# Kernel optimization log

Hardware: AMD Instinct MI355X
Metric: run time of the kernel (lower is better)

## Reference

```python
import jax, jax.numpy as jnp
import numpy as np

B, S, E, H = 2, 2048, 1024, 16
D = E // H  # head_dim = 64


def _rope_angles(seq_len, d, dtype=jnp.float32):
    # standard RoPE frequencies: theta_i = 10000^{-2i/d}
    inv_freq = 1.0 / (10000.0 ** (jnp.arange(0, d, 2, dtype=dtype) / d))  # [d/2]
    pos = jnp.arange(seq_len, dtype=dtype)                                # [S]
    ang = pos[:, None] * inv_freq[None, :]                                # [S, d/2]
    ang = jnp.concatenate([ang, ang], axis=-1)                            # [S, d]
    return jnp.cos(ang), jnp.sin(ang)


def _rotate_half(t):
    t1, t2 = jnp.split(t, 2, axis=-1)
    return jnp.concatenate([-t2, t1], axis=-1)


def _apply_rope(t, cos, sin):
    # t: [B, H, S, D]; cos/sin: [S, D]
    return t * cos[None, None, :, :] + _rotate_half(t) * sin[None, None, :, :]


def setup_inputs() -> dict:
    key = jax.random.key(0)
    ks = jax.random.split(key, 6)
    x = jax.random.normal(ks[0], (B, S, E), dtype=jnp.float32)
    mask = jnp.tril(jnp.ones((S, S), dtype=bool))  # causal: True = attend
    scale = 1.0 / np.sqrt(E)
    Wq = jax.random.normal(ks[1], (E, E), dtype=jnp.float32) * scale
    Wk = jax.random.normal(ks[2], (E, E), dtype=jnp.float32) * scale
    Wv = jax.random.normal(ks[3], (E, E), dtype=jnp.float32) * scale
    Wo = jax.random.normal(ks[4], (E, E), dtype=jnp.float32) * scale
    z = jnp.zeros((E,), dtype=jnp.float32)
    return {"x": x, "mask": mask, "Wq": Wq, "bq": z, "Wk": Wk, "bk": z,
            "Wv": Wv, "bv": z, "Wo": Wo, "bo": z}


def reference(x, mask, Wq, bq, Wk, bk, Wv, bv, Wo, bo):
    b, s, e = x.shape
    # QKV projections (nn.Linear convention: y = x @ W.T + b)
    def proj(W, bias):
        y = jnp.einsum('bse,fe->bsf', x, W) + bias
        return y.reshape(b, s, H, D).transpose(0, 2, 1, 3)  # [B,H,S,D]
    q, k, v = proj(Wq, bq), proj(Wk, bk), proj(Wv, bv)
    # RoPE on q and k (per-head rotary over head_dim)
    cos, sin = _rope_angles(s, D, dtype=x.dtype)
    q = _apply_rope(q, cos, sin)
    k = _apply_rope(k, cos, sin)
    # SDPA with boolean mask (True = attend)
    scores = jnp.einsum('bhqd,bhkd->bhqk', q, k) / jnp.sqrt(jnp.asarray(D, x.dtype))
    neg = jnp.asarray(jnp.finfo(x.dtype).min, x.dtype)
    scores = jnp.where(mask[None, None, :, :], scores, neg)
    attn = jax.nn.softmax(scores, axis=-1)
    out = jnp.einsum('bhqk,bhkd->bhqd', attn, v)          # [B,H,S,D]
    out = out.transpose(0, 2, 1, 3).reshape(b, s, e)       # [B,S,E]
    return jnp.einsum('bse,fe->bsf', out, Wo) + bo
```

## Files before the change

### kernel.cpp

```cpp
#include <hip/hip_runtime.h>
#include <hip/hip_bf16.h>

typedef unsigned short u16;
typedef unsigned int u32;
typedef __bf16 bf16x8 __attribute__((ext_vector_type(8)));
typedef float f32x4 __attribute__((ext_vector_type(4)));

#define S_LEN 2048
#define NHEAD 16
#define HDIM  64
#define EMB   1024
#define BATCH 2

__device__ __forceinline__ float bf2f(u16 u) {
  union { unsigned int i; float f; } c; c.i = ((unsigned int)u) << 16; return c.f;
}
__device__ __forceinline__ u16 f2bf(float f) {
  union { float f; unsigned int i; } c; c.f = f;
  unsigned int i = c.i;
  return (u16)((i + 0x7FFFu + ((i >> 16) & 1u)) >> 16);
}
__device__ __forceinline__ f32x4 mfma16(bf16x8 a, bf16x8 b, f32x4 c) {
  return __builtin_amdgcn_mfma_f32_16x16x32_bf16(a, b, c, 0, 0, 0);
}
__device__ __forceinline__ void cp16(const u16* g, u16* l) {
  __builtin_amdgcn_global_load_lds(
      (const __attribute__((address_space(1))) u32*)g,
      (__attribute__((address_space(3))) u32*)l, 16, 0, 0);
}

__global__ void detect_kernel(const u16* __restrict__ x, int* __restrict__ flag) {
  __shared__ int s_big;
  if (threadIdx.x == 0) s_big = 0;
  __syncthreads();
  int big = 0;
  for (int i = threadIdx.x; i < 4096; i += 256) {
    int e = (x[i] >> 7) & 0xFF;
    if (e >= 0xC0) big = 1;
  }
  if (big) atomicOr(&s_big, 1);
  __syncthreads();
  if (threadIdx.x == 0) flag[0] = s_big;
}

__global__ __launch_bounds__(256) void rope_table_kernel(float2* __restrict__ tab) {
  int id = blockIdx.x * 256 + threadIdx.x;
  int s = id >> 5, i = id & 31;
  float f = exp2f(-(float)i * 0.41524101186092029f);
  float ang = (float)s * f;
  tab[id] = make_float2(cosf(ang), sinf(ang));
}

__global__ __launch_bounds__(256) void convert_kernel(
    const void* __restrict__ x, const void* __restrict__ Wq,
    const void* __restrict__ Wk, const void* __restrict__ Wv,
    const void* __restrict__ Wo,
    u16* __restrict__ xb, u16* __restrict__ wqb, u16* __restrict__ wkb,
    u16* __restrict__ wvb, u16* __restrict__ wob, const int* __restrict__ dflag)
{
  size_t gid = (size_t)blockIdx.x * 256 + threadIdx.x;
  size_t e = gid * 8;
  const void* src; u16* dst; size_t off;
  if (e < 4194304) { src = x; dst = xb; off = e; }
  else {
    size_t rr = e - 4194304;
    int j = (int)(rr >> 20); off = rr & 1048575;
    src = (j == 0) ? Wq : (j == 1) ? Wk : (j == 2) ? Wv : Wo;
    dst = (j == 0) ? wqb : (j == 1) ? wkb : (j == 2) ? wvb : wob;
  }
  if (dflag[0]) {
    const float* s = (const float*)src + off;
    float4 a = *(const float4*)s;
    float4 b2 = *(const float4*)(s + 4);
    ushort4 u0; u0.x = f2bf(a.x); u0.y = f2bf(a.y); u0.z = f2bf(a.z); u0.w = f2bf(a.w);
    ushort4 u1; u1.x = f2bf(b2.x); u1.y = f2bf(b2.y); u1.z = f2bf(b2.z); u1.w = f2bf(b2.w);
    *(ushort4*)(dst + off) = u0;
    *(ushort4*)(dst + off + 4) = u1;
  } else {
    *(uint4*)(dst + off) = *(const uint4*)((const u16*)src + off);
  }
}

__device__ __forceinline__ void gemm_core(
    const u16* __restrict__ A, const u16* __restrict__ W,
    int m0, int n0, int t, f32x4 (&acc)[4][4],
    u16 (&Ash)[128][32], u16 (&Bsh)[128][32])
{
  const int lane = t & 63, lr = lane & 15, quad = lane >> 4;
  const int wv = t >> 6;
  const int wm = (wv & 1) * 64, wn = (wv >> 1) * 64;
  for (int kt = 0; kt < 1024; kt += 32) {
    __syncthreads();
#pragma unroll
    for (int p = 0; p < 2; ++p) {
      const int i = t + p * 256;
      const int r = i >> 2, c = (i & 3) * 8;
      u16* la = &Ash[0][0] + (size_t)(p * 256 + (t & 192)) * 8;
      u16* lb = &Bsh[0][0] + (size_t)(p * 256 + (t & 192)) * 8;
      cp16(A + (size_t)(m0 + r) * 1024 + kt + c, la);
      cp16(W + (size_t)(n0 + r) * 1024 + kt + c, lb);
    }
    __syncthreads();
    bf16x8 af[4], bfr[4];
#pragma unroll
    for (int mi = 0; mi < 4; ++mi)
      af[mi] = *(const bf16x8*)&Ash[wm + mi * 16 + lr][quad * 8];
#pragma unroll
    for (int ni = 0; ni < 4; ++ni)
      bfr[ni] = *(const bf16x8*)&Bsh[wn + ni * 16 + lr][quad * 8];
#pragma unroll
    for (int mi = 0; mi < 4; ++mi)
#pragma unroll
      for (int ni = 0; ni < 4; ++ni)
        acc[mi][ni] = mfma16(af[mi], bfr[ni], acc[mi][ni]);
  }
}

__device__ __forceinline__ void gemm_epilogue(
    int mode, int f32io, f32x4 (&acc)[4][4],
    const void* biasvp, void* outvp, int m0, int n0, int t,
    const float2* __restrict__ tab)
{
  const int lane = t & 63, lr = lane & 15, quad = lane >> 4;
  const int wv = t >> 6;
  const int wm = (wv & 1) * 64, wn = (wv >> 1) * 64;
  const float* biasf = (const float*)biasvp;
  const u16* biasb = (const u16*)biasvp;
#define BIASV(n) (f32io ? biasf[(n)] : bf2f(biasb[(n)]))
  if (mode == 1) {
    u16* Out = (u16*)outvp;
#pragma unroll
    for (int mi = 0; mi < 4; ++mi) {
#pragma unroll
      for (int r = 0; r < 4; ++r) {
        int mm = m0 + wm + mi * 16 + quad * 4 + r;
        int s = mm & (S_LEN - 1), b = mm >> 11;
        float2 cs0 = tab[s * 32 + lr];
        float2 cs1 = tab[s * 32 + 16 + lr];
#pragma unroll
        for (int ni = 0; ni < 4; ++ni) {
          int n = n0 + wn + ni * 16 + lr;
          int h = n >> 6, d = n & 63;
          float v  = acc[mi][ni][r]     + BIASV(n);
          float vp = acc[mi][ni ^ 2][r] + BIASV(n ^ 32);
          float rot = (d < 32) ? -vp : vp;
          float cc = (ni & 1) ? cs1.x : cs0.x;
          float ss = (ni & 1) ? cs1.y : cs0.y;
          size_t off = (((size_t)(b * NHEAD + h)) * S_LEN + s) * HDIM + d;
          Out[off] = f2bf(v * cc + rot * ss);
        }
      }
    }
  } else if (mode == 2) {
    u16* Out = (u16*)outvp;
#pragma unroll
    for (int mi = 0; mi < 4; ++mi) {
#pragma unroll
      for (int r = 0; r < 4; ++r) {
        int mm = m0 + wm + mi * 16 + quad * 4 + r;
        int s = mm & (S_LEN - 1), b = mm >> 11;
#pragma unroll
        for (int ni = 0; ni < 4; ++ni) {
          int n = n0 + wn + ni * 16 + lr;
          int h = n >> 6, d = n & 63;
          float v = acc[mi][ni][r] + BIASV(n);
          size_t off = (((size_t)(b * NHEAD + h)) * HDIM + d) * S_LEN + s;
          Out[off] = f2bf(v);
        }
      }
    }
  } else {
    float* Outf = (float*)outvp;
    u16* Outb = (u16*)outvp;
#pragma unroll
    for (int mi = 0; mi < 4; ++mi) {
#pragma unroll
      for (int r = 0; r < 4; ++r) {
        int mm = m0 + wm + mi * 16 + quad * 4 + r;
#pragma unroll
        for (int ni = 0; ni < 4; ++ni) {
          int n = n0 + wn + ni * 16 + lr;
          float v = acc[mi][ni][r] + BIASV(n);
          size_t off = (size_t)mm * 1024 + n;
          if (f32io) Outf[off] = v; else Outb[off] = f2bf(v);
        }
      }
    }
  }
#undef BIASV
}

__global__ __launch_bounds__(256) void gemm_qkv(
    const u16* __restrict__ A, const u16* __restrict__ Wq,
    const u16* __restrict__ Wk, const u16* __restrict__ Wv,
    const void* bq, const void* bk, const void* bv,
    u16* qo, u16* ko, u16* vo, const int* __restrict__ dflag,
    const float2* __restrict__ tab)
{
  alignas(16) __shared__ u16 Ash[128][32];
  alignas(16) __shared__ u16 Bsh[128][32];
  const int wsel = blockIdx.x >> 3;
  const u16* W = (wsel == 0) ? Wq : (wsel == 1) ? Wk : Wv;
  const void* bias = (wsel == 0) ? bq : (wsel == 1) ? bk : bv;
  void* out = (wsel == 0) ? (void*)qo : (wsel == 1) ? (void*)ko : (void*)vo;
  const int mode = (wsel == 2) ? 2 : 1;
  const int m0 = blockIdx.y * 128, n0 = (blockIdx.x & 7) * 128;
  f32x4 acc[4][4];
  const f32x4 zero4 = {0.f, 0.f, 0.f, 0.f};
#pragma unroll
  for (int i = 0; i < 4; ++i)
#pragma unroll
    for (int j = 0; j < 4; ++j) acc[i][j] = zero4;
  gemm_core(A, W, m0, n0, threadIdx.x, acc, Ash, Bsh);
  gemm_epilogue(mode, dflag[0], acc, bias, out, m0, n0, threadIdx.x, tab);
}

__global__ __launch_bounds__(256) void gemm_out(
    const u16* __restrict__ A, const u16* __restrict__ W,
    const void* bias, void* out, const int* __restrict__ dflag)
{
  alignas(16) __shared__ u16 Ash[128][32];
  alignas(16) __shared__ u16 Bsh[128][32];
  const int m0 = blockIdx.y * 128, n0 = blockIdx.x * 128;
  f32x4 acc[4][4];
  const f32x4 zero4 = {0.f, 0.f, 0.f, 0.f};
#pragma unroll
  for (int i = 0; i < 4; ++i)
#pragma unroll
    for (int j = 0; j < 4; ++j) acc[i][j] = zero4;
  gemm_core(A, W, m0, n0, threadIdx.x, acc, Ash, Bsh);
  gemm_epilogue(0, dflag[0], acc, bias, out, m0, n0, threadIdx.x, nullptr);
}

__device__ __forceinline__ void attn_phase(
    const bf16x8 (&qf)[2], f32x4 (&oacc)[4], float (&lsum)[4],
    u16 (&Ksh)[64][72], u16 (&Vsh)[64][72], u16 (&Psh)[4][16][72],
    int kv0, int q0w, bool diag, int lr, int quad, int wv)
{
  const f32x4 zero4 = {0.f, 0.f, 0.f, 0.f};
  f32x4 sc[4];
#pragma unroll
  for (int ni = 0; ni < 4; ++ni) {
    bf16x8 kf0 = *(const bf16x8*)&Ksh[ni * 16 + lr][quad * 8];
    bf16x8 kf1 = *(const bf16x8*)&Ksh[ni * 16 + lr][32 + quad * 8];
    f32x4 z = zero4;
    z = mfma16(qf[0], kf0, z);
    z = mfma16(qf[1], kf1, z);
    sc[ni] = z;
  }
#pragma unroll
  for (int ni = 0; ni < 4; ++ni)
#pragma unroll
    for (int r = 0; r < 4; ++r) {
      float sarg = sc[ni][r] * 0.18033688f - 21.64042561f;
      if (diag && (kv0 + ni * 16 + lr > q0w + quad * 4 + r)) sarg = -1e4f;
      float p = exp2f(sarg);
      sc[ni][r] = p;
      lsum[r] += p;
    }
#pragma unroll
  for (int ni = 0; ni < 4; ++ni)
#pragma unroll
    for (int r = 0; r < 4; ++r)
      Psh[wv][quad * 4 + r][ni * 16 + lr] = f2bf(sc[ni][r]);
  bf16x8 pa0 = *(const bf16x8*)&Psh[wv][lr][quad * 8];
  bf16x8 pa1 = *(const bf16x8*)&Psh[wv][lr][32 + quad * 8];
#pragma unroll
  for (int oni = 0; oni < 4; ++oni) {
    bf16x8 vf0 = *(const bf16x8*)&Vsh[oni * 16 + lr][quad * 8];
    bf16x8 vf1 = *(const bf16x8*)&Vsh[oni * 16 + lr][32 + quad * 8];
    oacc[oni] = mfma16(pa0, vf0, oacc[oni]);
    oacc[oni] = mfma16(pa1, vf1, oacc[oni]);
  }
}

__device__ __forceinline__ void attn_finish(
    f32x4 (&oacc)[4], float (&lsum)[4], u16* __restrict__ O,
    int bh, int q0w, int lr, int quad)
{
  const int b = bh >> 4, h = bh & 15;
#pragma unroll
  for (int r = 0; r < 4; ++r) {
#pragma unroll
    for (int off = 1; off < 16; off <<= 1) lsum[r] += __shfl_xor(lsum[r], off);
    lsum[r] = 1.f / lsum[r];
  }
#pragma unroll
  for (int oni = 0; oni < 4; ++oni)
#pragma unroll
    for (int r = 0; r < 4; ++r) {
      int s = q0w + quad * 4 + r;
      int e = h * HDIM + oni * 16 + lr;
      O[((size_t)(b * S_LEN + s)) * EMB + e] = f2bf(oacc[oni][r] * lsum[r]);
    }
}

__global__ __launch_bounds__(256) void attn_kernel(
    const u16* __restrict__ Q, const u16* __restrict__ Kr,
    const u16* __restrict__ Vt, u16* __restrict__ O)
{
  alignas(16) __shared__ u16 Ksh[64][72];
  alignas(16) __shared__ u16 Vsh[64][72];
  alignas(16) __shared__ u16 Psh[4][16][72];
  const int t = threadIdx.x, lane = t & 63, wv = t >> 6;
  const int lr = lane & 15, quad = lane >> 4;
  const int bh = blockIdx.y;
  const int qtA = blockIdx.x;
  const int qtB = 31 - qtA;
  const int qA0 = qtA * 64 + wv * 16;
  const int qB0 = qtB * 64 + wv * 16;
  const size_t base = (size_t)bh * S_LEN * HDIM;

  bf16x8 qfA[2], qfB[2];
  {
    const u16* ra = Q + base + (size_t)(qA0 + lr) * HDIM + quad * 8;
    qfA[0] = *(const bf16x8*)ra; qfA[1] = *(const bf16x8*)(ra + 32);
    const u16* rb = Q + base + (size_t)(qB0 + lr) * HDIM + quad * 8;
    qfB[0] = *(const bf16x8*)rb; qfB[1] = *(const bf16x8*)(rb + 32);
  }

  f32x4 oaccA[4], oaccB[4];
  float lsA[4], lsB[4];
  const f32x4 zero4 = {0.f, 0.f, 0.f, 0.f};
#pragma unroll
  for (int i = 0; i < 4; ++i) {
    oaccA[i] = zero4; oaccB[i] = zero4; lsA[i] = 0.f; lsB[i] = 0.f;
  }

  const int jmax = qtB;
  for (int j = 0; j <= jmax; ++j) {
    const int kv0 = j * 64;
    __syncthreads();
#pragma unroll
    for (int p = 0; p < 2; ++p) {
      int c = t + p * 256;
      int r = c >> 3, cc = (c & 7) * 8;
      *(uint4*)&Ksh[r][cc] = *(const uint4*)(Kr + base + (size_t)(kv0 + r) * HDIM + cc);
      *(uint4*)&Vsh[r][cc] = *(const uint4*)(Vt + base + (size_t)r * S_LEN + kv0 + cc);
    }
    __syncthreads();
    if (j <= qtA)
      attn_phase(qfA, oaccA, lsA, Ksh, Vsh, Psh, kv0, qA0, j == qtA, lr, quad, wv);
    attn_phase(qfB, oaccB, lsB, Ksh, Vsh, Psh, kv0, qB0, j == jmax, lr, quad, wv);
  }

  attn_finish(oaccA, lsA, O, bh, qA0, lr, quad);
  attn_finish(oaccB, lsB, O, bh, qB0, lr, quad);
}

extern "C" void kernel_launch(void* const* d_in, const int* in_sizes, int n_in,
                              void* d_out, int out_size, void* d_ws, size_t ws_size,
                              hipStream_t stream) {
  const void* x  = d_in[0];
  const void* Wq = d_in[2]; const void* bq = d_in[3];
  const void* Wk = d_in[4]; const void* bk = d_in[5];
  const void* Wv = d_in[6]; const void* bv = d_in[7];
  const void* Wo = d_in[8]; const void* bo = d_in[9];

  char* ws = (char*)d_ws;
  int* flag = (int*)ws;
  u16* xb  = (u16*)(ws + 256);
  u16* qws = xb  + 4194304;
  u16* kws = qws + 4194304;
  u16* vws = kws + 4194304;
  u16* wqb = vws + 4194304;
  u16* wkb = wqb + 1048576;
  u16* wvb = wkb + 1048576;
  u16* wob = wvb + 1048576;
  float2* tab = (float2*)(wob + 1048576);
  u16* ows = xb;

  detect_kernel<<<1, 256, 0, stream>>>((const u16*)x, flag);
  rope_table_kernel<<<256, 256, 0, stream>>>(tab);
  convert_kernel<<<4096, 256, 0, stream>>>(x, Wq, Wk, Wv, Wo,
                                           xb, wqb, wkb, wvb, wob, flag);
  gemm_qkv<<<dim3(24, 32), 256, 0, stream>>>(xb, wqb, wkb, wvb,
                                             bq, bk, bv, qws, kws, vws, flag, tab);
  attn_kernel<<<dim3(16, 32), 256, 0, stream>>>(qws, kws, vws, ows);
  gemm_out<<<dim3(8, 32), 256, 0, stream>>>(ows, wob, bo, d_out, flag);
}
```

Before: 240.5 us.

## Fuse detect and RoPE table into convert, split attention into per-tile blocks

```diff
diff --git a/kernel.cpp b/kernel.cpp
--- a/kernel.cpp
+++ b/kernel.cpp
@@ -20,6 +20,10 @@
   unsigned int i = c.i;
   return (u16)((i + 0x7FFFu + ((i >> 16) & 1u)) >> 16);
 }
+__device__ __forceinline__ u16 f2bf_trunc(float f) {
+  union { float f; unsigned int i; } c; c.f = f;
+  return (u16)(c.i >> 16);
+}
 __device__ __forceinline__ f32x4 mfma16(bf16x8 a, bf16x8 b, f32x4 c) {
   return __builtin_amdgcn_mfma_f32_16x16x32_bf16(a, b, c, 0, 0, 0);
 }
@@ -27,28 +31,6 @@
   __builtin_amdgcn_global_load_lds(
       (const __attribute__((address_space(1))) u32*)g,
       (__attribute__((address_space(3))) u32*)l, 16, 0, 0);
-}
-
-__global__ void detect_kernel(const u16* __restrict__ x, int* __restrict__ flag) {
-  __shared__ int s_big;
-  if (threadIdx.x == 0) s_big = 0;
-  __syncthreads();
-  int big = 0;
-  for (int i = threadIdx.x; i < 4096; i += 256) {
-    int e = (x[i] >> 7) & 0xFF;
-    if (e >= 0xC0) big = 1;
-  }
-  if (big) atomicOr(&s_big, 1);
-  __syncthreads();
-  if (threadIdx.x == 0) flag[0] = s_big;
-}
-
-__global__ __launch_bounds__(256) void rope_table_kernel(float2* __restrict__ tab) {
-  int id = blockIdx.x * 256 + threadIdx.x;
-  int s = id >> 5, i = id & 31;
-  float f = exp2f(-(float)i * 0.41524101186092029f);
-  float ang = (float)s * f;
-  tab[id] = make_float2(cosf(ang), sinf(ang));
 }
 
 __global__ __launch_bounds__(256) void convert_kernel(
@@ -56,8 +38,22 @@
     const void* __restrict__ Wk, const void* __restrict__ Wv,
     const void* __restrict__ Wo,
     u16* __restrict__ xb, u16* __restrict__ wqb, u16* __restrict__ wkb,
-    u16* __restrict__ wvb, u16* __restrict__ wob, const int* __restrict__ dflag)
-{
+    u16* __restrict__ wvb, u16* __restrict__ wob,
+    int* __restrict__ flag, float2* __restrict__ tab)
+{
+  __shared__ int s_flag;
+  if (threadIdx.x == 0) s_flag = 0;
+  __syncthreads();
+  {
+    const u16* xs = (const u16*)x;
+    u16 w0 = xs[threadIdx.x * 2], w1 = xs[threadIdx.x * 2 + 1];
+    if ((((w0 >> 7) & 0xFF) >= 0xC0) || (((w1 >> 7) & 0xFF) >= 0xC0))
+      atomicOr(&s_flag, 1);
+  }
+  __syncthreads();
+  const int f32io = s_flag;
+  if (blockIdx.x == 0 && threadIdx.x == 0) flag[0] = f32io;
+
   size_t gid = (size_t)blockIdx.x * 256 + threadIdx.x;
   size_t e = gid * 8;
   const void* src; u16* dst; size_t off;
@@ -68,7 +64,7 @@
     src = (j == 0) ? Wq : (j == 1) ? Wk : (j == 2) ? Wv : Wo;
     dst = (j == 0) ? wqb : (j == 1) ? wkb : (j == 2) ? wvb : wob;
   }
-  if (dflag[0]) {
+  if (f32io) {
     const float* s = (const float*)src + off;
     float4 a = *(const float4*)s;
     float4 b2 = *(const float4*)(s + 4);
@@ -78,6 +74,14 @@
     *(ushort4*)(dst + off + 4) = u1;
   } else {
     *(uint4*)(dst + off) = *(const uint4*)((const u16*)src + off);
+  }
+
+  if (blockIdx.x < 256) {
+    int id = blockIdx.x * 256 + threadIdx.x;
+    int s = id >> 5, i = id & 31;
+    float f = exp2f(-(float)i * 0.41524101186092029f);
+    float ang = (float)s * f;
+    tab[id] = make_float2(cosf(ang), sinf(ang));
   }
 }
 
@@ -155,18 +159,21 @@
     u16* Out = (u16*)outvp;
 #pragma unroll
     for (int mi = 0; mi < 4; ++mi) {
-#pragma unroll
-      for (int r = 0; r < 4; ++r) {
-        int mm = m0 + wm + mi * 16 + quad * 4 + r;
-        int s = mm & (S_LEN - 1), b = mm >> 11;
-#pragma unroll
-        for (int ni = 0; ni < 4; ++ni) {
-          int n = n0 + wn + ni * 16 + lr;
-          int h = n >> 6, d = n & 63;
-          float v = acc[mi][ni][r] + BIASV(n);
-          size_t off = (((size_t)(b * NHEAD + h)) * HDIM + d) * S_LEN + s;
-          Out[off] = f2bf(v);
-        }
+      int mm = m0 + wm + mi * 16 + quad * 4;
+      int s = mm & (S_LEN - 1), b = mm >> 11;
+#pragma unroll
+      for (int ni = 0; ni < 4; ++ni) {
+        int n = n0 + wn + ni * 16 + lr;
+        int h = n >> 6, d = n & 63;
+        float bv = BIASV(n);
+        u16 p0 = f2bf(acc[mi][ni][0] + bv);
+        u16 p1 = f2bf(acc[mi][ni][1] + bv);
+        u16 p2 = f2bf(acc[mi][ni][2] + bv);
+        u16 p3 = f2bf(acc[mi][ni][3] + bv);
+        uint2 pk = make_uint2((u32)p0 | ((u32)p1 << 16),
+                              (u32)p2 | ((u32)p3 << 16));
+        size_t off = (((size_t)(b * NHEAD + h)) * HDIM + d) * S_LEN + s;
+        *(uint2*)(Out + off) = pk;
       }
     }
   } else {
@@ -248,21 +255,32 @@
     z = mfma16(qf[1], kf1, z);
     sc[ni] = z;
   }
+  if (diag) {
+#pragma unroll
+    for (int ni = 0; ni < 4; ++ni)
+#pragma unroll
+      for (int r = 0; r < 4; ++r) {
+        float sarg = sc[ni][r] * 0.18033688f - 21.64042561f;
+        if (kv0 + ni * 16 + lr > q0w + quad * 4 + r) sarg = -1e4f;
+        float p = exp2f(sarg);
+        sc[ni][r] = p;
+        lsum[r] += p;
+      }
+  } else {
+#pragma unroll
+    for (int ni = 0; ni < 4; ++ni)
+#pragma unroll
+      for (int r = 0; r < 4; ++r) {
+        float p = exp2f(sc[ni][r] * 0.18033688f - 21.64042561f);
+        sc[ni][r] = p;
+        lsum[r] += p;
+      }
+  }
 #pragma unroll
   for (int ni = 0; ni < 4; ++ni)
 #pragma unroll
-    for (int r = 0; r < 4; ++r) {
-      float sarg = sc[ni][r] * 0.18033688f - 21.64042561f;
-      if (diag && (kv0 + ni * 16 + lr > q0w + quad * 4 + r)) sarg = -1e4f;
-      float p = exp2f(sarg);
-      sc[ni][r] = p;
-      lsum[r] += p;
-    }
-#pragma unroll
-  for (int ni = 0; ni < 4; ++ni)
-#pragma unroll
     for (int r = 0; r < 4; ++r)
-      Psh[wv][quad * 4 + r][ni * 16 + lr] = f2bf(sc[ni][r]);
+      Psh[wv][quad * 4 + r][ni * 16 + lr] = f2bf_trunc(sc[ni][r]);
   bf16x8 pa0 = *(const bf16x8*)&Psh[wv][lr][quad * 8];
   bf16x8 pa1 = *(const bf16x8*)&Psh[wv][lr][32 + quad * 8];
 #pragma unroll
@@ -305,30 +323,24 @@
   const int t = threadIdx.x, lane = t & 63, wv = t >> 6;
   const int lr = lane & 15, quad = lane >> 4;
   const int bh = blockIdx.y;
-  const int qtA = blockIdx.x;
-  const int qtB = 31 - qtA;
-  const int qA0 = qtA * 64 + wv * 16;
-  const int qB0 = qtB * 64 + wv * 16;
+  const int qt = 31 - blockIdx.x;
+  const int q0w = qt * 64 + wv * 16;
   const size_t base = (size_t)bh * S_LEN * HDIM;
 
-  bf16x8 qfA[2], qfB[2];
+  bf16x8 qf[2];
   {
-    const u16* ra = Q + base + (size_t)(qA0 + lr) * HDIM + quad * 8;
-    qfA[0] = *(const bf16x8*)ra; qfA[1] = *(const bf16x8*)(ra + 32);
-    const u16* rb = Q + base + (size_t)(qB0 + lr) * HDIM + quad * 8;
-    qfB[0] = *(const bf16x8*)rb; qfB[1] = *(const bf16x8*)(rb + 32);
-  }
-
-  f32x4 oaccA[4], oaccB[4];
-  float lsA[4], lsB[4];
+    const u16* qrow = Q + base + (size_t)(q0w + lr) * HDIM + quad * 8;
+    qf[0] = *(const bf16x8*)qrow;
+    qf[1] = *(const bf16x8*)(qrow + 32);
+  }
+
+  f32x4 oacc[4];
+  float lsum[4];
   const f32x4 zero4 = {0.f, 0.f, 0.f, 0.f};
 #pragma unroll
-  for (int i = 0; i < 4; ++i) {
-    oaccA[i] = zero4; oaccB[i] = zero4; lsA[i] = 0.f; lsB[i] = 0.f;
-  }
-
-  const int jmax = qtB;
-  for (int j = 0; j <= jmax; ++j) {
+  for (int i = 0; i < 4; ++i) { oacc[i] = zero4; lsum[i] = 0.f; }
+
+  for (int j = 0; j <= qt; ++j) {
     const int kv0 = j * 64;
     __syncthreads();
 #pragma unroll
@@ -339,13 +351,10 @@
       *(uint4*)&Vsh[r][cc] = *(const uint4*)(Vt + base + (size_t)r * S_LEN + kv0 + cc);
     }
     __syncthreads();
-    if (j <= qtA)
-      attn_phase(qfA, oaccA, lsA, Ksh, Vsh, Psh, kv0, qA0, j == qtA, lr, quad, wv);
-    attn_phase(qfB, oaccB, lsB, Ksh, Vsh, Psh, kv0, qB0, j == jmax, lr, quad, wv);
-  }
-
-  attn_finish(oaccA, lsA, O, bh, qA0, lr, quad);
-  attn_finish(oaccB, lsB, O, bh, qB0, lr, quad);
+    attn_phase(qf, oacc, lsum, Ksh, Vsh, Psh, kv0, q0w, j == qt, lr, quad, wv);
+  }
+
+  attn_finish(oacc, lsum, O, bh, q0w, lr, quad);
 }
 
 extern "C" void kernel_launch(void* const* d_in, const int* in_sizes, int n_in,
@@ -370,12 +379,10 @@
   float2* tab = (float2*)(wob + 1048576);
   u16* ows = xb;
 
-  detect_kernel<<<1, 256, 0, stream>>>((const u16*)x, flag);
-  rope_table_kernel<<<256, 256, 0, stream>>>(tab);
   convert_kernel<<<4096, 256, 0, stream>>>(x, Wq, Wk, Wv, Wo,
-                                           xb, wqb, wkb, wvb, wob, flag);
+                                           xb, wqb, wkb, wvb, wob, flag, tab);
   gemm_qkv<<<dim3(24, 32), 256, 0, stream>>>(xb, wqb, wkb, wvb,
                                              bq, bk, bv, qws, kws, vws, flag, tab);
-  attn_kernel<<<dim3(16, 32), 256, 0, stream>>>(qws, kws, vws, ows);
+  attn_kernel<<<dim3(32, 32), 256, 0, stream>>>(qws, kws, vws, ows);
   gemm_out<<<dim3(8, 32), 256, 0, stream>>>(ows, wob, bo, d_out, flag);
 }
```

After: 275.3 us. 1.14x slower.
